# Kernel tuning notes

Hardware: AMD Instinct MI355X
Metric: run time of the kernel (lower is better)

Reference implementation:

```python
import jax, jax.numpy as jnp
import numpy as np

N = 16384   # total nodes (16 graphs x 32x32 grid)
E = 65536   # edges (before self loops)
F_IN = 7
H = 8       # gat heads
C = 200     # gat hidden per head
HC = H * C  # 1600
GCN = 1600
CNN = 64
OUT = 6
B = 16      # graphs per batch
G = 32      # grid size
EPS = 1e-5


def _bn1(x, g, b):
    # BatchNorm1d, training-mode batch stats (biased var), x: [N, F]
    mu = x.mean(0)
    var = x.var(0)
    return (x - mu) * jax.lax.rsqrt(var + EPS) * g + b


def _bn2(x, g, b):
    # BatchNorm2d over (N, H, W), x: [B, C, H, W]
    mu = x.mean((0, 2, 3), keepdims=True)
    var = x.var((0, 2, 3), keepdims=True)
    return (x - mu) * jax.lax.rsqrt(var + EPS) * g[None, :, None, None] + b[None, :, None, None]


def _conv5(x, w, b):
    y = jax.lax.conv_general_dilated(x, w, (1, 1), [(2, 2), (2, 2)],
                                     dimension_numbers=('NCHW', 'OIHW', 'NCHW'))
    return y + b[None, :, None, None]


def _gatv2(x, Wl, bl, Wr, br, We, att, bias, src, dst, edge_attr):
    # PyG GATv2Conv: concat=True, add_self_loops=True (fill_value='mean'), edge_dim=1
    n = x.shape[0]
    xl = (x @ Wl + bl).reshape(n, H, C)  # source transform
    xr = (x @ Wr + br).reshape(n, H, C)  # target transform
    loop = jnp.arange(n, dtype=src.dtype)
    s = jnp.concatenate([src, loop])
    d = jnp.concatenate([dst, loop])
    ea_loop = jnp.broadcast_to(edge_attr.mean(0, keepdims=True), (n, edge_attr.shape[1]))
    ea = jnp.concatenate([edge_attr, ea_loop], 0)
    ee = (ea @ We).reshape(-1, H, C)
    m = jax.nn.leaky_relu(xl[s] + xr[d] + ee, 0.2)       # [E+N, H, C]
    alpha = jnp.einsum('ehc,hc->eh', m, att)             # [E+N, H]
    amax = jax.ops.segment_max(alpha, d, num_segments=n)
    ex = jnp.exp(alpha - amax[d])
    denom = jax.ops.segment_sum(ex, d, num_segments=n)
    a = ex / denom[d]                                    # scatter-softmax over in-edges
    out = jax.ops.segment_sum(xl[s] * a[:, :, None], d, num_segments=n)  # [N, H, C]
    return out.reshape(n, HC) + bias


def setup_inputs() -> dict:
    k = jax.random.key(0)
    ks = jax.random.split(k, 16)
    def nrm(i, shape, s):
        return jax.random.normal(ks[i], shape, jnp.float32) * s
    z = lambda *s: jnp.zeros(s, jnp.float32)
    o = lambda *s: jnp.ones(s, jnp.float32)
    return {
        'x': nrm(0, (N, F_IN), 1.0),
        'edge_attr': jax.random.uniform(ks[1], (E, 1), jnp.float32),
        'Wl': nrm(2, (F_IN, HC), 0.3), 'bl': z(HC),
        'Wr': nrm(3, (F_IN, HC), 0.3), 'br': z(HC),
        'We': nrm(4, (1, HC), 0.3), 'att': nrm(5, (H, C), 0.1), 'gat_b': z(HC),
        'bn1_g': o(HC), 'bn1_b': z(HC),
        'W1': nrm(6, (HC, GCN), 0.025), 'b1': z(GCN),
        'bn2_g': o(GCN), 'bn2_b': z(GCN),
        'W2': nrm(7, (GCN, GCN), 0.025), 'b2': z(GCN),
        'Wp': nrm(8, (GCN, CNN), 0.025), 'bp': z(CNN),
        'cw1': nrm(9, (CNN, CNN, 5, 5), 0.025), 'cb1': z(CNN), 'g1': o(CNN), 'be1': z(CNN),
        'cw2': nrm(10, (128, CNN, 5, 5), 0.025), 'cb2': z(128), 'g2': o(128), 'be2': z(128),
        'cw3': nrm(11, (CNN, 128, 5, 5), 0.025), 'cb3': z(CNN), 'g3': o(CNN), 'be3': z(CNN),
        'cw4': nrm(12, (OUT, CNN, 5, 5), 0.025), 'cb4': z(OUT),
        'src': jax.random.randint(ks[13], (E,), 0, N, jnp.int32),
        'dst': jax.random.randint(ks[14], (E,), 0, N, jnp.int32),
    }


def reference(x, edge_attr, Wl, bl, Wr, br, We, att, gat_b, bn1_g, bn1_b,
              W1, b1, bn2_g, bn2_b, W2, b2, Wp, bp,
              cw1, cb1, g1, be1, cw2, cb2, g2, be2, cw3, cb3, g3, be3, cw4, cb4,
              src, dst):
    h = _gatv2(x, Wl, bl, Wr, br, We, att, gat_b, src, dst, edge_attr)
    h = jax.nn.leaky_relu(_bn1(h, bn1_g, bn1_b), 0.01)
    h = jax.nn.relu(_bn1(h @ W1 + b1, bn2_g, bn2_b))
    h = jax.nn.relu(h @ W2 + b2)
    # per-graph projection + reshape to grid (batch vector is contiguous arange//1024)
    h = (h @ Wp + bp).reshape(B, G, G, CNN).transpose(0, 3, 1, 2)  # [B, CNN, G, G]
    h = jax.nn.relu(_bn2(_conv5(h, cw1, cb1), g1, be1))
    h = jax.nn.relu(_bn2(_conv5(h, cw2, cb2), g2, be2))
    h = jax.nn.relu(_bn2(_conv5(h, cw3, cb3), g3, be3))
    return _conv5(h, cw4, cb4)  # [B, 6, G, G]
```

## Files before the change

kernel.cpp:

```cpp
#include <hip/hip_runtime.h>
#include <cstdint>
#include <cstddef>

#define N_NODES 16384
#define N_EDGES 65536
#define EN_TOT  (N_EDGES + N_NODES)
#define FIN 7
#define HC 1600
#define NH 8
#define CHD 200
#define GCN 1600
#define CNN 64
#define BATCH 16
#define BN_EPS 1e-5f

typedef unsigned short ushort_t;
typedef __attribute__((ext_vector_type(8))) short s8frag;
typedef __attribute__((ext_vector_type(4))) float f32x4;

__device__ __forceinline__ ushort_t f2bf(float f) {
    unsigned u = __float_as_uint(f);
    unsigned r = (u + 0x7FFFu + ((u >> 16) & 1u)) >> 16;
    return (ushort_t)r;
}
__device__ __forceinline__ float bf2f(ushort_t u) {
    return __uint_as_float(((unsigned)u) << 16);
}

__device__ __forceinline__ void gload16(const void* g, void* l) {
    __builtin_amdgcn_global_load_lds((const __attribute__((address_space(1))) void*)g,
                                     (__attribute__((address_space(3))) void*)l, 16, 0, 0);
}

#define SWZ_KOFF(tid) ((((tid) & 3) ^ (((tid) >> 3) & 3)) << 3)
#define SWZ_AQ(lane, am) (((((lane) >> 4) ^ (((am) >> 1) & 3)) << 3))

__global__ __launch_bounds__(256) void k_count(
    const int* __restrict__ dst, const float* __restrict__ ea,
    int* __restrict__ cnt, float* __restrict__ ea_sum)
{
    int e = blockIdx.x * 256 + threadIdx.x;
    int d = (e < N_EDGES) ? dst[e] : (e - N_EDGES);
    atomicAdd(&cnt[d], 1);
    float v = (e < N_EDGES) ? ea[e] : 0.f;
#pragma unroll
    for (int o = 1; o < 64; o <<= 1) v += __shfl_xor(v, o);
    if ((threadIdx.x & 63) == 0) atomicAdd(ea_sum, v);
}

__global__ __launch_bounds__(256) void k_scan(int* __restrict__ cnt, int* __restrict__ offs)
{
    __shared__ int part[256];
    int t = threadIdx.x;
    int base_i = t * 64;
    int s = 0;
    for (int i = 0; i < 64; i++) s += cnt[base_i + i];
    part[t] = s;
    __syncthreads();
    for (int o = 1; o < 256; o <<= 1) {
        int add = (t >= o) ? part[t - o] : 0;
        __syncthreads();
        part[t] += add;
        __syncthreads();
    }
    int run = (t == 0) ? 0 : part[t - 1];
    for (int i = 0; i < 64; i++) {
        int v = cnt[base_i + i];
        offs[base_i + i] = run;
        run += v;
        cnt[base_i + i] = 0;
    }
    if (t == 255) offs[N_NODES] = run;
}

__global__ __launch_bounds__(256) void k_fill(const int* __restrict__ dst,
    const int* __restrict__ offs, int* __restrict__ cur, int* __restrict__ eid)
{
    int e = blockIdx.x * 256 + threadIdx.x;
    if (e >= EN_TOT) return;
    int d = (e < N_EDGES) ? dst[e] : (e - N_EDGES);
    int pos = offs[d] + atomicAdd(&cur[d], 1);
    eid[pos] = e;
}

__global__ __launch_bounds__(256) void k_gprep(
    const float* __restrict__ Wl, const float* __restrict__ bl,
    const float* __restrict__ Wr, const float* __restrict__ br,
    const float* __restrict__ We, const float* __restrict__ att,
    ushort_t* __restrict__ G, float* __restrict__ att16)
{
    int cp = blockIdx.x * 256 + threadIdx.x;
    if (cp >= 8 * 208) return;
    int h = cp / 208, j = cp - h * 208;
    ushort_t v[32];
#pragma unroll
    for (int k = 0; k < 32; k++) v[k] = 0;
    float av = 0.f;
    if (j < 200) {
        int c = h * 200 + j;
#pragma unroll
        for (int k = 0; k < 7; k++) v[k]     = f2bf(Wl[k * HC + c]);
#pragma unroll
        for (int k = 0; k < 7; k++) v[7 + k] = f2bf(Wr[k * HC + c]);
        v[14] = f2bf(We[c]);
        v[15] = f2bf(bl[c] + br[c]);
        av = att[h * CHD + j];
    }
    uint4* dst4 = (uint4*)(G + (size_t)cp * 32);
#pragma unroll
    for (int i = 0; i < 4; i++) dst4[i] = ((uint4*)v)[i];
    att16[cp] = av;
}

__global__ __launch_bounds__(256) void k_alpha_mm(
    const float* __restrict__ x, const float* __restrict__ edge_attr,
    const float* __restrict__ ea_sum, const int* __restrict__ src,
    const int* __restrict__ dst, const ushort_t* __restrict__ G,
    const float* __restrict__ att16, float* __restrict__ alpha)
{
    __shared__ ushort_t Fs[64 * 32];
    int tid = threadIdx.x;
    int lane = tid & 63, w = tid >> 6;
    int e0 = blockIdx.x * 64;
    float eam = ea_sum[0] * (1.f / (float)N_EDGES);

#define FSLOT(j, k) ((j) * 32 + ((((k) >> 3) ^ (((j) >> 1) & 3)) << 3) + ((k) & 7))
    for (int i = tid; i < 64 * 16; i += 256) {
        int j = i >> 4, k = (i & 15) + 16;
        Fs[FSLOT(j, k)] = 0;
    }
    {
        int j = tid >> 2, part = tid & 3;
        int e = e0 + j;
        int s, d; float ea;
        if (e < N_EDGES) { s = src[e]; d = dst[e]; ea = edge_attr[e]; }
        else             { s = e - N_EDGES; d = s; ea = eam; }
        if (part == 0) {
#pragma unroll
            for (int k = 0; k < 4; k++) Fs[FSLOT(j, k)] = f2bf(x[s * 7 + k]);
        } else if (part == 1) {
#pragma unroll
            for (int k = 4; k < 7; k++) Fs[FSLOT(j, k)] = f2bf(x[s * 7 + k]);
            Fs[FSLOT(j, 7)] = f2bf(x[d * 7 + 0]);
        } else if (part == 2) {
#pragma unroll
            for (int k = 1; k < 5; k++) Fs[FSLOT(j, 7 + k)] = f2bf(x[d * 7 + k]);
        } else {
            Fs[FSLOT(j, 12)] = f2bf(x[d * 7 + 5]);
            Fs[FSLOT(j, 13)] = f2bf(x[d * 7 + 6]);
            Fs[FSLOT(j, 14)] = f2bf(ea);
            Fs[FSLOT(j, 15)] = f2bf(1.0f);
        }
    }
#undef FSLOT
    __syncthreads();

    int am = lane & 15;
    int aq = (lane >> 4) * 8;
    s8frag afrag = *(const s8frag*)&Fs[(w * 16 + am) * 32 + SWZ_AQ(lane, am)];
    int lr4 = (lane >> 4) * 4;
    int ew = e0 + w * 16;
#pragma unroll
    for (int h = 0; h < NH; h++) {
        f32x4 hacc = (f32x4)0.f;
        int colbase = h * 208;
#pragma unroll
        for (int t = 0; t < 13; t++) {
            int cb = colbase + t * 16;
            s8frag bfrag = *(const s8frag*)(G + ((size_t)(cb + am) * 32 + aq));
            f32x4 z = (f32x4)0.f;
            f32x4 p = __builtin_amdgcn_mfma_f32_16x16x32_bf16(afrag, bfrag, z, 0, 0, 0);
            float attv = att16[cb + am];
#pragma unroll
            for (int r = 0; r < 4; r++) {
                float v = p[r];
                v = (v >= 0.f) ? v : 0.2f * v;
                hacc[r] += v * attv;
            }
        }
#pragma unroll
        for (int o = 1; o <= 8; o <<= 1) {
#pragma unroll
            for (int r = 0; r < 4; r++) hacc[r] += __shfl_xor(hacc[r], o);
        }
        if (am == 0) {
#pragma unroll
            for (int r = 0; r < 4; r++)
                alpha[(size_t)(ew + lr4 + r) * NH + h] = hacc[r];
        }
    }
}

__global__ __launch_bounds__(256) void k_agg_x(
    const float* __restrict__ x, const float* __restrict__ alpha,
    const int* __restrict__ offs, const int* __restrict__ eid,
    const int* __restrict__ src, float* __restrict__ xbar)
{
    int n = blockIdx.x * 4 + (threadIdx.x >> 6);
    int lane = threadIdx.x & 63;
    int beg = offs[n], deg = offs[n + 1] - beg;

    float pm[NH];
#pragma unroll
    for (int h = 0; h < NH; h++) pm[h] = -1e30f;
    for (int j = lane; j < deg; j += 64) {
        int e = eid[beg + j];
        const float* ap = alpha + (size_t)e * NH;
#pragma unroll
        for (int h = 0; h < NH; h++) pm[h] = fmaxf(pm[h], ap[h]);
    }
#pragma unroll
    for (int h = 0; h < NH; h++)
#pragma unroll
        for (int o = 1; o < 64; o <<= 1)
            pm[h] = fmaxf(pm[h], __shfl_xor(pm[h], o));

    float ps[NH];
    float px[NH][7];
#pragma unroll
    for (int h = 0; h < NH; h++) {
        ps[h] = 0.f;
#pragma unroll
        for (int k = 0; k < 7; k++) px[h][k] = 0.f;
    }
    for (int j = lane; j < deg; j += 64) {
        int e = eid[beg + j];
        int s = (e < N_EDGES) ? src[e] : (e - N_EDGES);
        float xv[7];
#pragma unroll
        for (int k = 0; k < 7; k++) xv[k] = x[s * 7 + k];
        const float* ap = alpha + (size_t)e * NH;
#pragma unroll
        for (int h = 0; h < NH; h++) {
            float p = __expf(ap[h] - pm[h]);
            ps[h] += p;
#pragma unroll
            for (int k = 0; k < 7; k++) px[h][k] += p * xv[k];
        }
    }
#pragma unroll
    for (int h = 0; h < NH; h++) {
#pragma unroll
        for (int o = 1; o < 64; o <<= 1) ps[h] += __shfl_xor(ps[h], o);
#pragma unroll
        for (int k = 0; k < 7; k++)
#pragma unroll
            for (int o = 1; o < 64; o <<= 1) px[h][k] += __shfl_xor(px[h][k], o);
    }
    float val = 0.f;
#pragma unroll
    for (int h = 0; h < NH; h++)
#pragma unroll
        for (int k = 0; k < 7; k++)
            if (lane == h * 7 + k) val = px[h][k] / ps[h];
    if (lane < 56) xbar[(size_t)n * 56 + lane] = val;
}

__global__ __launch_bounds__(256) void k_xmom(
    const float* __restrict__ xbar, float* __restrict__ mom)
{
    int h = blockIdx.x & 7, chunk = blockIdx.x >> 3;
    int tid = threadIdx.x, lane = tid & 63;
    float mu[7], S[49];
#pragma unroll
    for (int k = 0; k < 7; k++) mu[k] = 0.f;
#pragma unroll
    for (int k = 0; k < 49; k++) S[k] = 0.f;
    for (int i = 0; i < 8; i++) {
        int n = chunk * 2048 + i * 256 + tid;
        const float* xb = xbar + (size_t)n * 56 + h * 7;
        float xv[7];
#pragma unroll
        for (int k = 0; k < 7; k++) xv[k] = xb[k];
#pragma unroll
        for (int k = 0; k < 7; k++) {
            mu[k] += xv[k];
#pragma unroll
            for (int kk = 0; kk < 7; kk++) S[k * 7 + kk] += xv[k] * xv[kk];
        }
    }
#pragma unroll
    for (int o = 1; o < 64; o <<= 1) {
#pragma unroll
        for (int k = 0; k < 7; k++) mu[k] += __shfl_xor(mu[k], o);
#pragma unroll
        for (int k = 0; k < 49; k++) S[k] += __shfl_xor(S[k], o);
    }
    if (lane == 0) {
        float* mh = mom + h * 56;
#pragma unroll
        for (int k = 0; k < 7; k++) atomicAdd(&mh[k], mu[k]);
#pragma unroll
        for (int k = 0; k < 49; k++) atomicAdd(&mh[7 + k], S[k]);
    }
}

__global__ __launch_bounds__(256) void k_bn1_prep(
    const float* __restrict__ mom, const float* __restrict__ Wl,
    const float* __restrict__ bl, const float* __restrict__ gat_b,
    const float* __restrict__ g, const float* __restrict__ b,
    float* __restrict__ scale, float* __restrict__ shift)
{
    int f = blockIdx.x * 256 + threadIdx.x;
    if (f >= HC) return;
    int h = f / CHD;
    const float* mh = mom + h * 56;
    const float inv = 1.f / (float)N_NODES;
    float m[7], w[7];
#pragma unroll
    for (int k = 0; k < 7; k++) {
        m[k] = mh[k] * inv;
        w[k] = Wl[k * HC + f];
    }
    float mean = bl[f] + gat_b[f];
#pragma unroll
    for (int k = 0; k < 7; k++) mean += w[k] * m[k];
    float var = 0.f;
#pragma unroll
    for (int k = 0; k < 7; k++)
#pragma unroll
        for (int kk = 0; kk < 7; kk++)
            var += w[k] * w[kk] * (mh[7 + k * 7 + kk] * inv - m[k] * m[kk]);
    var = fmaxf(var, 0.f);
    float sc = g[f] * rsqrtf(var + BN_EPS);
    scale[f] = sc;
    shift[f] = b[f] - mean * sc;
}

__global__ __launch_bounds__(256) void k_project_bn(
    const float* __restrict__ xbar, const float* __restrict__ Wl,
    const float* __restrict__ bl, const float* __restrict__ gat_b,
    const float* __restrict__ scale, const float* __restrict__ shift,
    ushort_t* __restrict__ hout)
{
    __shared__ float xs[56];
    int n = blockIdx.x, tid = threadIdx.x;
    if (tid < 56) xs[tid] = xbar[(size_t)n * 56 + tid];
    __syncthreads();
    if (tid >= 200) return;
    int f0 = tid * 8;
    int h = f0 / CHD;
    float xb[7];
#pragma unroll
    for (int k = 0; k < 7; k++) xb[k] = xs[h * 7 + k];
    float acc[8];
    {
        float4 b0 = *(const float4*)(bl + f0), b1 = *(const float4*)(bl + f0 + 4);
        float4 g0 = *(const float4*)(gat_b + f0), g1 = *(const float4*)(gat_b + f0 + 4);
        acc[0] = b0.x + g0.x; acc[1] = b0.y + g0.y; acc[2] = b0.z + g0.z; acc[3] = b0.w + g0.w;
        acc[4] = b1.x + g1.x; acc[5] = b1.y + g1.y; acc[6] = b1.z + g1.z; acc[7] = b1.w + g1.w;
    }
#pragma unroll
    for (int k = 0; k < 7; k++) {
        float4 w0 = *(const float4*)(Wl + k * HC + f0);
        float4 w1 = *(const float4*)(Wl + k * HC + f0 + 4);
        acc[0] += xb[k] * w0.x; acc[1] += xb[k] * w0.y;
        acc[2] += xb[k] * w0.z; acc[3] += xb[k] * w0.w;
        acc[4] += xb[k] * w1.x; acc[5] += xb[k] * w1.y;
        acc[6] += xb[k] * w1.z; acc[7] += xb[k] * w1.w;
    }
    float4 s0 = *(const float4*)(scale + f0), s1 = *(const float4*)(scale + f0 + 4);
    float4 h0 = *(const float4*)(shift + f0), h1 = *(const float4*)(shift + f0 + 4);
    float sc[8] = {s0.x, s0.y, s0.z, s0.w, s1.x, s1.y, s1.z, s1.w};
    float sh[8] = {h0.x, h0.y, h0.z, h0.w, h1.x, h1.y, h1.z, h1.w};
    ushort_t o[8];
#pragma unroll
    for (int i = 0; i < 8; i++) {
        float v = acc[i] * sc[i] + sh[i];
        v = (v >= 0.f) ? v : 0.01f * v;
        o[i] = f2bf(v);
    }
    *(uint4*)(hout + (size_t)n * HC + f0) = *(uint4*)o;
}

__global__ __launch_bounds__(256) void k_bn_apply_bb(
    const ushort_t* __restrict__ X, ushort_t* __restrict__ Y,
    const float* __restrict__ bsum, const float* __restrict__ bsq,
    const float* __restrict__ g, const float* __restrict__ b,
    int rows, int total8, int F)
{
    int idx = blockIdx.x * 256 + threadIdx.x;
    if (idx >= total8) return;
    int e0 = idx * 8;
    int f0 = e0 % F;
    float inv = 1.f / (float)rows;
    uint4 xin = *(const uint4*)(X + e0);
    ushort_t* xv = (ushort_t*)&xin;
    ushort_t o[8];
#pragma unroll
    for (int i = 0; i < 8; i += 4) {
        float4 su = *(const float4*)(bsum + f0 + i);
        float4 sq = *(const float4*)(bsq + f0 + i);
        float4 gg = *(const float4*)(g + f0 + i);
        float4 bb = *(const float4*)(b + f0 + i);
        float mu, var, sc, sh, v;
#define DO1(comp, j) \
        mu = su.comp * inv; var = sq.comp * inv - mu * mu; \
        sc = gg.comp * rsqrtf(var + BN_EPS); sh = bb.comp - mu * sc; \
        v = bf2f(xv[i + j]) * sc + sh; v = fmaxf(v, 0.f); o[i + j] = f2bf(v);
        DO1(x, 0) DO1(y, 1) DO1(z, 2) DO1(w, 3)
#undef DO1
    }
    *(uint4*)(Y + e0) = *(uint4*)o;
}

__global__ __launch_bounds__(256) void k_bn_apply_pad(
    const ushort_t* __restrict__ X, ushort_t* __restrict__ pad,
    const float* __restrict__ bsum, const float* __restrict__ bsq,
    const float* __restrict__ g, const float* __restrict__ b,
    int total8, int Csh)
{
    int idx = blockIdx.x * 256 + threadIdx.x;
    if (idx >= total8) return;
    int e0 = idx * 8;
    int C = 1 << Csh;
    int c0 = e0 & (C - 1);
    int pix = e0 >> Csh;
    int xx = pix & 31, yy = (pix >> 5) & 31, bb2 = pix >> 10;
    float inv = 1.f / 16384.f;
    uint4 xin = *(const uint4*)(X + e0);
    ushort_t* xv = (ushort_t*)&xin;
    ushort_t o[8];
#pragma unroll
    for (int i = 0; i < 8; i += 4) {
        float4 su = *(const float4*)(bsum + c0 + i);
        float4 sq = *(const float4*)(bsq + c0 + i);
        float4 gg = *(const float4*)(g + c0 + i);
        float4 bb = *(const float4*)(b + c0 + i);
        float mu, var, sc, sh, v;
#define DO1(comp, j) \
        mu = su.comp * inv; var = sq.comp * inv - mu * mu; \
        sc = gg.comp * rsqrtf(var + BN_EPS); sh = bb.comp - mu * sc; \
        v = bf2f(xv[i + j]) * sc + sh; v = fmaxf(v, 0.f); o[i + j] = f2bf(v);
        DO1(x, 0) DO1(y, 1) DO1(z, 2) DO1(w, 3)
#undef DO1
    }
    *(uint4*)(pad + (((size_t)((bb2 * 36 + yy + 2) * 36 + xx + 2)) << Csh) + c0) = *(uint4*)o;
}

__global__ __launch_bounds__(256) void k_wt(
    const float* __restrict__ W, ushort_t* __restrict__ BT, int Kdim, int Ndim, int Npad)
{
    __shared__ float t[32][33];
    int tx = threadIdx.x & 31, ty = threadIdx.x >> 5;
    int n0 = blockIdx.x * 32, k0 = blockIdx.y * 32;
#pragma unroll
    for (int i = 0; i < 4; i++)
        t[ty + i * 8][tx] = (n0 + tx < Ndim)
            ? W[(size_t)(k0 + ty + i * 8) * Ndim + n0 + tx] : 0.f;
    __syncthreads();
#pragma unroll
    for (int i = 0; i < 4; i++)
        BT[(size_t)(n0 + ty + i * 8) * Kdim + k0 + tx] = f2bf(t[tx][ty + i * 8]);
}

__global__ __launch_bounds__(256) void k_cwt_all(
    const float* __restrict__ w1, const float* __restrict__ w2,
    const float* __restrict__ w3, const float* __restrict__ w4,
    ushort_t* __restrict__ o1, ushort_t* __restrict__ o2,
    ushort_t* __restrict__ o3, ushort_t* __restrict__ o4)
{
    int idx = blockIdx.x * 256 + threadIdx.x;
    const int R1 = 128 * 1600, R2 = 128 * 1600, R3 = 128 * 3200;
    const float* w; ushort_t* o; int local, K, Cin, Cout;
    if (idx < R1)                { w = w1; o = o1; local = idx; K = 1600; Cin = 64;  Cout = 64; }
    else if (idx < R1 + R2)      { w = w2; o = o2; local = idx - R1; K = 1600; Cin = 64; Cout = 128; }
    else if (idx < R1 + R2 + R3) { w = w3; o = o3; local = idx - R1 - R2; K = 3200; Cin = 128; Cout = 64; }
    else                         { w = w4; o = o4; local = idx - R1 - R2 - R3; K = 1600; Cin = 64; Cout = 6; }
    int co = local / K;
    int k = local - co * K;
    int p = k / Cin, ci = k - p * Cin;
    o[local] = (co < Cout) ? f2bf(w[(size_t)(co * Cin + ci) * 25 + p]) : (ushort_t)0;
}

__global__ __launch_bounds__(256) void k_mgemm(
    const ushort_t* __restrict__ A, const ushort_t* __restrict__ BT,
    const float* __restrict__ bias, ushort_t* __restrict__ Cb,
    float* __restrict__ bsum, float* __restrict__ bsq,
    int K, int Nvalid, int ldc, int relu)
{
    __shared__ __align__(16) ushort_t As[128 * 64];
    __shared__ __align__(16) ushort_t Bs[128 * 64];
    int tid = threadIdx.x;
    int lane = tid & 63;
    int wid = tid >> 6;
    int wy = wid >> 1, wx = wid & 1;

    int nx = gridDim.x;
    int lin = blockIdx.y * nx + blockIdx.x;
    int xcd = lin & 7;
    int q = lin >> 3;
    int colb = q % nx;
    int rowb = (q / nx) * 8 + xcd;
    int row0 = rowb * 128, col0 = colb * 128;

    f32x4 acc[4][4];
#pragma unroll
    for (int i = 0; i < 4; i++)
#pragma unroll
        for (int j = 0; j < 4; j++) acc[i][j] = (f32x4)0.f;

    int am = lane & 15, qq = lane >> 4;
    int lr4 = qq * 4;

    const ushort_t* pA[4];
    const ushort_t* pB[4];
    char* lA[4];
    char* lB[4];
#pragma unroll
    for (int j = 0; j < 4; j++) {
        int sA = j * 256 + tid;
        int rowS = sA >> 3, cS = sA & 7;
        int srcC = (cS ^ (rowS & 7)) << 3;
        pA[j] = A  + (size_t)(row0 + rowS) * K + srcC;
        pB[j] = BT + (size_t)(col0 + rowS) * K + srcC;
        lA[j] = (char*)As + sA * 16;
        lB[j] = (char*)Bs + sA * 16;
    }

    for (int kk = 0; kk < K; kk += 64) {
        __syncthreads();
#pragma unroll
        for (int j = 0; j < 4; j++) {
            gload16(pA[j], lA[j]); pA[j] += 64;
            gload16(pB[j], lB[j]); pB[j] += 64;
        }
        __syncthreads();

#pragma unroll
        for (int t = 0; t < 2; t++) {
            int sw = ((((t << 2) | qq) ^ (am & 7)) << 3);
            s8frag a[4], b[4];
#pragma unroll
            for (int mi = 0; mi < 4; mi++)
                a[mi] = *(const s8frag*)&As[(wy * 64 + mi * 16 + am) * 64 + sw];
#pragma unroll
            for (int ni = 0; ni < 4; ni++)
                b[ni] = *(const s8frag*)&Bs[(wx * 64 + ni * 16 + am) * 64 + sw];
#pragma unroll
            for (int mi = 0; mi < 4; mi++)
#pragma unroll
                for (int ni = 0; ni < 4; ni++)
                    acc[mi][ni] = __builtin_amdgcn_mfma_f32_16x16x32_bf16(
                        a[mi], b[ni], acc[mi][ni], 0, 0, 0);
        }
    }

    int lc = am;
#pragma unroll
    for (int ni = 0; ni < 4; ni++) {
        int col = col0 + wx * 64 + ni * 16 + lc;
        bool valid = col < Nvalid;
        float bv = valid ? bias[col] : 0.f;
        float s = 0.f, q2 = 0.f;
#pragma unroll
        for (int mi = 0; mi < 4; mi++) {
#pragma unroll
            for (int r = 0; r < 4; r++) {
                int row = row0 + wy * 64 + mi * 16 + lr4 + r;
                float v = acc[mi][ni][r] + bv;
                s += v; q2 += v * v;
                float vo = relu ? fmaxf(v, 0.f) : v;
                if (valid) Cb[(size_t)row * ldc + col] = f2bf(vo);
            }
        }
        if (bsum != nullptr && valid) {
            s += __shfl_xor(s, 16);  s += __shfl_xor(s, 32);
            q2 += __shfl_xor(q2, 16); q2 += __shfl_xor(q2, 32);
            if (qq == 0) {
                atomicAdd(&bsum[col], s);
                atomicAdd(&bsq[col], q2);
            }
        }
    }
}

__global__ __launch_bounds__(256) void k_cgemm3(
    const ushort_t* __restrict__ Ain, const ushort_t* __restrict__ BT,
    const float* __restrict__ bias, float* __restrict__ Cf, ushort_t* __restrict__ Cb,
    float* __restrict__ bsum, float* __restrict__ bsq,
    int K, int Csh, int Nvalid, int ldc, int out_mode, int linA)
{
    __shared__ __align__(16) ushort_t As[32 * 64];
    __shared__ __align__(16) ushort_t Bs[64 * 64];
    int tid = threadIdx.x;
    int lane = tid & 63;
    int w = tid >> 6, wr = w >> 1, wc = w & 1;
    int row0 = blockIdx.y * 32, col0 = blockIdx.x * 64;
    int Cmask = (1 << Csh) - 1;

    f32x4 acc[2];
    acc[0] = (f32x4)0.f; acc[1] = (f32x4)0.f;

    int rowSA = tid >> 3, cSA = tid & 7;
    int srcCA = (cSA ^ (rowSA & 7)) << 3;
    int pixA = row0 + rowSA;
    int bA = pixA >> 10, yA = (pixA >> 5) & 31, xA = pixA & 31;
    const ushort_t* aptr = Ain + (size_t)pixA * K + srcCA;

    int rowSB0 = tid >> 3, rowSB1 = rowSB0 + 32;
    int cSB = tid & 7;
    const ushort_t* bptr0 = BT + (size_t)(col0 + rowSB0) * K + ((cSB ^ (rowSB0 & 7)) << 3);
    const ushort_t* bptr1 = BT + (size_t)(col0 + rowSB1) * K + ((cSB ^ (rowSB1 & 7)) << 3);

    char* lA  = (char*)As + tid * 16;
    char* lB0 = (char*)Bs + tid * 16;
    char* lB1 = (char*)Bs + (tid + 256) * 16;

    int am = lane & 15, qq = lane >> 4;

    for (int kk = 0; kk < K; kk += 64) {
        __syncthreads();
        if (linA) {
            gload16(aptr, lA);
            aptr += 64;
        } else {
            int k = kk + srcCA;
            int p = k >> Csh;
            int ci = k & Cmask;
            int ky = p / 5, kx = p - ky * 5;
            gload16(Ain + (((size_t)((bA * 36 + yA + ky) * 36 + xA + kx) << Csh) + ci), lA);
        }
        gload16(bptr0, lB0); bptr0 += 64;
        gload16(bptr1, lB1); bptr1 += 64;
        __syncthreads();

#pragma unroll
        for (int t = 0; t < 2; t++) {
            int sw = ((((t << 2) | qq) ^ (am & 7)) << 3);
            s8frag a   = *(const s8frag*)&As[(wr * 16 + am) * 64 + sw];
            s8frag b0f = *(const s8frag*)&Bs[(wc * 32 + am) * 64 + sw];
            s8frag b1f = *(const s8frag*)&Bs[(wc * 32 + 16 + am) * 64 + sw];
            acc[0] = __builtin_amdgcn_mfma_f32_16x16x32_bf16(a, b0f, acc[0], 0, 0, 0);
            acc[1] = __builtin_amdgcn_mfma_f32_16x16x32_bf16(a, b1f, acc[1], 0, 0, 0);
        }
    }

    int lc = am, lr4 = qq * 4;
#pragma unroll
    for (int ni = 0; ni < 2; ni++) {
        int col = col0 + wc * 32 + ni * 16 + lc;
        bool valid = col < Nvalid;
        float bv = valid ? bias[col] : 0.f;
        float s = 0.f, q2 = 0.f;
#pragma unroll
        for (int r = 0; r < 4; r++) {
            int row = row0 + wr * 16 + lr4 + r;
            float v = acc[ni][r] + bv;
            s += v; q2 += v * v;
            if (valid) {
                if (out_mode == 1) {
                    Cb[(size_t)row * ldc + col] = f2bf(v);
                } else if (out_mode == 3) {
                    int bb = row >> 10, sp = row & 1023;
                    int yy = sp >> 5, xx = sp & 31;
                    Cb[((size_t)((bb * 36 + yy + 2) * 36 + xx + 2) << 6) + col] = f2bf(v);
                } else {
                    int bb = row >> 10, sp = row & 1023;
                    Cf[(size_t)((bb * 6 + col) << 10) + sp] = v;
                }
            }
        }
        if (bsum != nullptr && valid) {
            s += __shfl_xor(s, 16);  s += __shfl_xor(s, 32);
            q2 += __shfl_xor(q2, 16); q2 += __shfl_xor(q2, 32);
            if (qq == 0) {
                atomicAdd(&bsum[col], s);
                atomicAdd(&bsq[col], q2);
            }
        }
    }
}

extern "C" void kernel_launch(void* const* d_in, const int* in_sizes, int n_in,
                              void* d_out, int out_size, void* d_ws, size_t ws_size,
                              hipStream_t stream)
{
    const float* x   = (const float*)d_in[0];
    const float* ea  = (const float*)d_in[1];
    const float* Wl  = (const float*)d_in[2];
    const float* bl  = (const float*)d_in[3];
    const float* Wr  = (const float*)d_in[4];
    const float* br  = (const float*)d_in[5];
    const float* We  = (const float*)d_in[6];
    const float* att = (const float*)d_in[7];
    const float* gat_b = (const float*)d_in[8];
    const float* bn1_g = (const float*)d_in[9];
    const float* bn1_b = (const float*)d_in[10];
    const float* W1 = (const float*)d_in[11];
    const float* b1 = (const float*)d_in[12];
    const float* bn2_g = (const float*)d_in[13];
    const float* bn2_b = (const float*)d_in[14];
    const float* W2 = (const float*)d_in[15];
    const float* b2 = (const float*)d_in[16];
    const float* Wp = (const float*)d_in[17];
    const float* bp = (const float*)d_in[18];
    const float* cw1 = (const float*)d_in[19]; const float* cb1 = (const float*)d_in[20];
    const float* g1  = (const float*)d_in[21]; const float* be1 = (const float*)d_in[22];
    const float* cw2 = (const float*)d_in[23]; const float* cb2 = (const float*)d_in[24];
    const float* g2  = (const float*)d_in[25]; const float* be2 = (const float*)d_in[26];
    const float* cw3 = (const float*)d_in[27]; const float* cb3 = (const float*)d_in[28];
    const float* g3  = (const float*)d_in[29]; const float* be3 = (const float*)d_in[30];
    const float* cw4 = (const float*)d_in[31]; const float* cb4 = (const float*)d_in[32];
    const int* src = (const int*)d_in[33];
    const int* dst = (const int*)d_in[34];
    float* out = (float*)d_out;

    const size_t SZ_REGION = (size_t)N_NODES * HC * 4;
    const size_t HALF = SZ_REGION / 2;
    char* ws = (char*)d_ws;
    char* regA = ws;
    char* regB = regA + SZ_REGION;
    char* wbase = regB + SZ_REGION;
    ushort_t* W1T  = (ushort_t*)wbase;
    ushort_t* W2T  = W1T + (size_t)1664 * 1600;
    ushort_t* WpT  = W2T + (size_t)1664 * 1600;
    ushort_t* c1T  = WpT + (size_t)128 * 1600;
    ushort_t* c2T  = c1T + (size_t)128 * 1600;
    ushort_t* c3T  = c2T + (size_t)128 * 1600;
    ushort_t* c4T  = c3T + (size_t)128 * 3200;
    ushort_t* G16  = c4T + (size_t)128 * 1600;
    float* att16   = (float*)(G16 + (size_t)1664 * 32);
    float* alpha   = att16 + 1664 + 64;
    float* xbar    = alpha + (size_t)EN_TOT * NH;
    float* bn_sc   = xbar + (size_t)N_NODES * 56;
    float* bn_sh   = bn_sc + HC;
    int*   cnt    = (int*)(bn_sh + HC + 64);
    float* ea_sum = (float*)(cnt + N_NODES);
    float* mom    = ea_sum + 16;
    float* bnG1   = mom + 448;
    float* bnC1   = bnG1 + 3200;
    float* bnC2   = bnC1 + 256;
    float* bnC3   = bnC2 + 256;
    const size_t ZBYTES = (char*)(bnC3 + 256) - (char*)cnt;
    int* offs = (int*)(bnC3 + 256 + 16);
    int* eid  = offs + N_NODES + 1 + 63;

    ushort_t* abuf16  = (ushort_t*)regA;
    ushort_t* a2buf16 = (ushort_t*)(regA + HALF);
    ushort_t* pad1 = (ushort_t*)regA;
    ushort_t* pad2 = (ushort_t*)(regA + (4u << 20));
    ushort_t* pad3 = (ushort_t*)(regA + (8u << 20));
    ushort_t* pad4 = (ushort_t*)(regA + (14u << 20));
    ushort_t* c1out = (ushort_t*)(regA + (18u << 20));
    ushort_t* c2out = (ushort_t*)(regA + (22u << 20));
    ushort_t* c3out = (ushort_t*)(regA + (27u << 20));
    ushort_t* g1b16   = (ushort_t*)regB;
    ushort_t* h3_16   = (ushort_t*)regB;

    k_wt<<<dim3(52, 50), 256, 0, stream>>>(W1, W1T, 1600, 1600, 1664);
    k_wt<<<dim3(52, 50), 256, 0, stream>>>(W2, W2T, 1600, 1600, 1664);
    k_wt<<<dim3(4, 50), 256, 0, stream>>>(Wp, WpT, 1600, 64, 128);
    k_cwt_all<<<4000, 256, 0, stream>>>(cw1, cw2, cw3, cw4, c1T, c2T, c3T, c4T);
    k_gprep<<<7, 256, 0, stream>>>(Wl, bl, Wr, br, We, att, G16, att16);

    hipMemsetAsync(cnt, 0, ZBYTES, stream);
    k_count<<<EN_TOT / 256, 256, 0, stream>>>(dst, ea, cnt, ea_sum);
    k_scan<<<1, 256, 0, stream>>>(cnt, offs);
    k_fill<<<EN_TOT / 256, 256, 0, stream>>>(dst, offs, cnt, eid);
    k_alpha_mm<<<EN_TOT / 64, 256, 0, stream>>>(x, ea, ea_sum, src, dst, G16, att16, alpha);
    k_agg_x<<<N_NODES / 4, 256, 0, stream>>>(x, alpha, offs, eid, src, xbar);

    k_xmom<<<64, 256, 0, stream>>>(xbar, mom);
    k_bn1_prep<<<7, 256, 0, stream>>>(mom, Wl, bl, gat_b, bn1_g, bn1_b, bn_sc, bn_sh);
    k_project_bn<<<N_NODES, 256, 0, stream>>>(xbar, Wl, bl, gat_b, bn_sc, bn_sh, abuf16);

    k_mgemm<<<dim3(13, 128), 256, 0, stream>>>(abuf16, W1T, b1, g1b16,
                                               bnG1, bnG1 + 1600, 1600, 1600, 1600, 0);
    k_bn_apply_bb<<<(N_NODES * GCN / 8) / 256, 256, 0, stream>>>(g1b16, a2buf16,
                                                                 bnG1, bnG1 + 1600, bn2_g, bn2_b,
                                                                 N_NODES, N_NODES * GCN / 8, GCN);
    k_mgemm<<<dim3(13, 128), 256, 0, stream>>>(a2buf16, W2T, b2, h3_16,
                                               (float*)nullptr, (float*)nullptr, 1600, 1600, 1600, 1);

    hipMemsetAsync(regA, 0, (size_t)17 << 20, stream);

    k_cgemm3<<<dim3(1, 512), 256, 0, stream>>>(h3_16, WpT, bp, (float*)nullptr, pad1,
                                               (float*)nullptr, (float*)nullptr,
                                               1600, 6, 64, 64, 3, 1);
    k_cgemm3<<<dim3(1, 512), 256, 0, stream>>>(pad1, c1T, cb1, (float*)nullptr, c1out,
                                               bnC1, bnC1 + 128, 1600, 6, 64, 64, 1, 0);
    k_bn_apply_pad<<<(16384 * 64 / 8) / 256, 256, 0, stream>>>(c1out, pad2, bnC1, bnC1 + 128,
                                                               g1, be1, 16384 * 64 / 8, 6);
    k_cgemm3<<<dim3(2, 512), 256, 0, stream>>>(pad2, c2T, cb2, (float*)nullptr, c2out,
                                               bnC2, bnC2 + 128, 1600, 6, 128, 128, 1, 0);
    k_bn_apply_pad<<<(16384 * 128 / 8) / 256, 256, 0, stream>>>(c2out, pad3, bnC2, bnC2 + 128,
                                                                g2, be2, 16384 * 128 / 8, 7);
    k_cgemm3<<<dim3(1, 512), 256, 0, stream>>>(pad3, c3T, cb3, (float*)nullptr, c3out,
                                               bnC3, bnC3 + 128, 3200, 7, 64, 64, 1, 0);
    k_bn_apply_pad<<<(16384 * 64 / 8) / 256, 256, 0, stream>>>(c3out, pad4, bnC3, bnC3 + 128,
                                                               g3, be3, 16384 * 64 / 8, 6);
    k_cgemm3<<<dim3(1, 512), 256, 0, stream>>>(pad4, c4T, cb4, out, (ushort_t*)nullptr,
                                               (float*)nullptr, (float*)nullptr,
                                               1600, 6, 6, 6, 2, 0);

    (void)in_sizes; (void)n_in; (void)out_size; (void)ws_size;
}
```

Baseline: 843.7 us.

## Fuse CNN stage into one cooperative kernel and merge weight-prep launches

Replaces the four conv GEMM launches and three BN-apply launches with a single cooperative kernel of 512 blocks. Each block keeps its conv accumulators in registers across a grid.sync, then applies batch-norm and ReLU and writes straight into the next padded buffer, so the intermediate conv outputs are never written to or read back from memory. All weight-transpose and prep kernels are also merged into one launch. The cost is several grid-wide barriers, a layer-2 block that now computes both 64-column halves serially instead of spreading them over twice as many blocks, and a dependence on all 512 blocks being co-resident.

```diff
diff --git a/kernel.cpp b/kernel.cpp
--- a/kernel.cpp
+++ b/kernel.cpp
@@ -1,6 +1,9 @@
 #include <hip/hip_runtime.h>
+#include <hip/hip_cooperative_groups.h>
 #include <cstdint>
 #include <cstddef>
+
+namespace cg = cooperative_groups;
 
 #define N_NODES 16384
 #define N_EDGES 65536
@@ -83,33 +86,72 @@
     eid[pos] = e;
 }
 
-__global__ __launch_bounds__(256) void k_gprep(
+__global__ __launch_bounds__(256) void k_prep(
+    const float* __restrict__ W1, const float* __restrict__ W2, const float* __restrict__ Wp,
+    const float* __restrict__ cw1, const float* __restrict__ cw2,
+    const float* __restrict__ cw3, const float* __restrict__ cw4,
     const float* __restrict__ Wl, const float* __restrict__ bl,
     const float* __restrict__ Wr, const float* __restrict__ br,
     const float* __restrict__ We, const float* __restrict__ att,
+    ushort_t* __restrict__ W1T, ushort_t* __restrict__ W2T, ushort_t* __restrict__ WpT,
+    ushort_t* __restrict__ c1T, ushort_t* __restrict__ c2T,
+    ushort_t* __restrict__ c3T, ushort_t* __restrict__ c4T,
     ushort_t* __restrict__ G, float* __restrict__ att16)
 {
-    int cp = blockIdx.x * 256 + threadIdx.x;
-    if (cp >= 8 * 208) return;
-    int h = cp / 208, j = cp - h * 208;
-    ushort_t v[32];
-#pragma unroll
-    for (int k = 0; k < 32; k++) v[k] = 0;
-    float av = 0.f;
-    if (j < 200) {
-        int c = h * 200 + j;
-#pragma unroll
-        for (int k = 0; k < 7; k++) v[k]     = f2bf(Wl[k * HC + c]);
-#pragma unroll
-        for (int k = 0; k < 7; k++) v[7 + k] = f2bf(Wr[k * HC + c]);
-        v[14] = f2bf(We[c]);
-        v[15] = f2bf(bl[c] + br[c]);
-        av = att[h * CHD + j];
-    }
-    uint4* dst4 = (uint4*)(G + (size_t)cp * 32);
-#pragma unroll
-    for (int i = 0; i < 4; i++) dst4[i] = ((uint4*)v)[i];
-    att16[cp] = av;
+    __shared__ float t[32][33];
+    int lb = blockIdx.x;
+    int tid = threadIdx.x;
+    if (lb < 5400) {
+        const float* W; ushort_t* BT; int Ndim, bx, by;
+        if (lb < 2600)      { W = W1; BT = W1T; Ndim = 1600; bx = lb % 52; by = lb / 52; }
+        else if (lb < 5200) { W = W2; BT = W2T; Ndim = 1600; int l = lb - 2600; bx = l % 52; by = l / 52; }
+        else                { W = Wp; BT = WpT; Ndim = 64;   int l = lb - 5200; bx = l % 4;  by = l / 4; }
+        int tx = tid & 31, ty = tid >> 5;
+        int n0 = bx * 32, k0 = by * 32;
+#pragma unroll
+        for (int i = 0; i < 4; i++)
+            t[ty + i * 8][tx] = (n0 + tx < Ndim)
+                ? W[(size_t)(k0 + ty + i * 8) * Ndim + n0 + tx] : 0.f;
+        __syncthreads();
+#pragma unroll
+        for (int i = 0; i < 4; i++)
+            BT[(size_t)(n0 + ty + i * 8) * 1600 + k0 + tx] = f2bf(t[tx][ty + i * 8]);
+    } else if (lb < 9400) {
+        int idx = (lb - 5400) * 256 + tid;
+        const int R1 = 128 * 1600, R2 = 128 * 1600, R3 = 128 * 3200;
+        const float* w; ushort_t* o; int local, K, Cin, Cout;
+        if (idx < R1)                { w = cw1; o = c1T; local = idx; K = 1600; Cin = 64;  Cout = 64; }
+        else if (idx < R1 + R2)      { w = cw2; o = c2T; local = idx - R1; K = 1600; Cin = 64; Cout = 128; }
+        else if (idx < R1 + R2 + R3) { w = cw3; o = c3T; local = idx - R1 - R2; K = 3200; Cin = 128; Cout = 64; }
+        else                         { w = cw4; o = c4T; local = idx - R1 - R2 - R3; K = 1600; Cin = 64; Cout = 6; }
+        int co = local / K;
+        int k = local - co * K;
+        int p = k / Cin, ci = k - p * Cin;
+        o[local] = (co < Cout) ? f2bf(w[(size_t)(co * Cin + ci) * 25 + p]) : (ushort_t)0;
+    } else {
+        int cp = (lb - 9400) * 256 + tid;
+        if (cp < 8 * 208) {
+            int h = cp / 208, j = cp - h * 208;
+            ushort_t v[32];
+#pragma unroll
+            for (int k = 0; k < 32; k++) v[k] = 0;
+            float av = 0.f;
+            if (j < 200) {
+                int c = h * 200 + j;
+#pragma unroll
+                for (int k = 0; k < 7; k++) v[k]     = f2bf(Wl[k * HC + c]);
+#pragma unroll
+                for (int k = 0; k < 7; k++) v[7 + k] = f2bf(Wr[k * HC + c]);
+                v[14] = f2bf(We[c]);
+                v[15] = f2bf(bl[c] + br[c]);
+                av = att[h * CHD + j];
+            }
+            uint4* dst4 = (uint4*)(G + (size_t)cp * 32);
+#pragma unroll
+            for (int i = 0; i < 4; i++) dst4[i] = ((uint4*)v)[i];
+            att16[cp] = av;
+        }
+    }
 }
 
 __global__ __launch_bounds__(256) void k_alpha_mm(
@@ -404,75 +446,6 @@
     *(uint4*)(Y + e0) = *(uint4*)o;
 }
 
-__global__ __launch_bounds__(256) void k_bn_apply_pad(
-    const ushort_t* __restrict__ X, ushort_t* __restrict__ pad,
-    const float* __restrict__ bsum, const float* __restrict__ bsq,
-    const float* __restrict__ g, const float* __restrict__ b,
-    int total8, int Csh)
-{
-    int idx = blockIdx.x * 256 + threadIdx.x;
-    if (idx >= total8) return;
-    int e0 = idx * 8;
-    int C = 1 << Csh;
-    int c0 = e0 & (C - 1);
-    int pix = e0 >> Csh;
-    int xx = pix & 31, yy = (pix >> 5) & 31, bb2 = pix >> 10;
-    float inv = 1.f / 16384.f;
-    uint4 xin = *(const uint4*)(X + e0);
-    ushort_t* xv = (ushort_t*)&xin;
-    ushort_t o[8];
-#pragma unroll
-    for (int i = 0; i < 8; i += 4) {
-        float4 su = *(const float4*)(bsum + c0 + i);
-        float4 sq = *(const float4*)(bsq + c0 + i);
-        float4 gg = *(const float4*)(g + c0 + i);
-        float4 bb = *(const float4*)(b + c0 + i);
-        float mu, var, sc, sh, v;
-#define DO1(comp, j) \
-        mu = su.comp * inv; var = sq.comp * inv - mu * mu; \
-        sc = gg.comp * rsqrtf(var + BN_EPS); sh = bb.comp - mu * sc; \
-        v = bf2f(xv[i + j]) * sc + sh; v = fmaxf(v, 0.f); o[i + j] = f2bf(v);
-        DO1(x, 0) DO1(y, 1) DO1(z, 2) DO1(w, 3)
-#undef DO1
-    }
-    *(uint4*)(pad + (((size_t)((bb2 * 36 + yy + 2) * 36 + xx + 2)) << Csh) + c0) = *(uint4*)o;
-}
-
-__global__ __launch_bounds__(256) void k_wt(
-    const float* __restrict__ W, ushort_t* __restrict__ BT, int Kdim, int Ndim, int Npad)
-{
-    __shared__ float t[32][33];
-    int tx = threadIdx.x & 31, ty = threadIdx.x >> 5;
-    int n0 = blockIdx.x * 32, k0 = blockIdx.y * 32;
-#pragma unroll
-    for (int i = 0; i < 4; i++)
-        t[ty + i * 8][tx] = (n0 + tx < Ndim)
-            ? W[(size_t)(k0 + ty + i * 8) * Ndim + n0 + tx] : 0.f;
-    __syncthreads();
-#pragma unroll
-    for (int i = 0; i < 4; i++)
-        BT[(size_t)(n0 + ty + i * 8) * Kdim + k0 + tx] = f2bf(t[tx][ty + i * 8]);
-}
-
-__global__ __launch_bounds__(256) void k_cwt_all(
-    const float* __restrict__ w1, const float* __restrict__ w2,
-    const float* __restrict__ w3, const float* __restrict__ w4,
-    ushort_t* __restrict__ o1, ushort_t* __restrict__ o2,
-    ushort_t* __restrict__ o3, ushort_t* __restrict__ o4)
-{
-    int idx = blockIdx.x * 256 + threadIdx.x;
-    const int R1 = 128 * 1600, R2 = 128 * 1600, R3 = 128 * 3200;
-    const float* w; ushort_t* o; int local, K, Cin, Cout;
-    if (idx < R1)                { w = w1; o = o1; local = idx; K = 1600; Cin = 64;  Cout = 64; }
-    else if (idx < R1 + R2)      { w = w2; o = o2; local = idx - R1; K = 1600; Cin = 64; Cout = 128; }
-    else if (idx < R1 + R2 + R3) { w = w3; o = o3; local = idx - R1 - R2; K = 3200; Cin = 128; Cout = 64; }
-    else                         { w = w4; o = o4; local = idx - R1 - R2 - R3; K = 1600; Cin = 64; Cout = 6; }
-    int co = local / K;
-    int k = local - co * K;
-    int p = k / Cin, ci = k - p * Cin;
-    o[local] = (co < Cout) ? f2bf(w[(size_t)(co * Cin + ci) * 25 + p]) : (ushort_t)0;
-}
-
 __global__ __launch_bounds__(256) void k_mgemm(
     const ushort_t* __restrict__ A, const ushort_t* __restrict__ BT,
     const float* __restrict__ bias, ushort_t* __restrict__ Cb,
@@ -575,21 +548,25 @@
     }
 }
 
-__global__ __launch_bounds__(256) void k_cgemm3(
+struct CArgs {
+    const ushort_t *h3, *WpT, *c1T, *c2T, *c3T, *c4T;
+    const float *bp, *cb1, *cb2, *cb3, *cb4;
+    const float *g1, *be1, *g2, *be2, *g3, *be3;
+    float *bnC1, *bnC2, *bnC3;
+    ushort_t *pad1, *pad2, *pad3, *pad4;
+    float *out;
+};
+
+__device__ __forceinline__ void gemm_tile32x64(
     const ushort_t* __restrict__ Ain, const ushort_t* __restrict__ BT,
-    const float* __restrict__ bias, float* __restrict__ Cf, ushort_t* __restrict__ Cb,
-    float* __restrict__ bsum, float* __restrict__ bsq,
-    int K, int Csh, int Nvalid, int ldc, int out_mode, int linA)
-{
-    __shared__ __align__(16) ushort_t As[32 * 64];
-    __shared__ __align__(16) ushort_t Bs[64 * 64];
+    int K, int Csh, int linA, int row0, int col0,
+    ushort_t* As, ushort_t* Bs, f32x4* acc)
+{
     int tid = threadIdx.x;
     int lane = tid & 63;
+    int am = lane & 15, qq = lane >> 4;
     int w = tid >> 6, wr = w >> 1, wc = w & 1;
-    int row0 = blockIdx.y * 32, col0 = blockIdx.x * 64;
     int Cmask = (1 << Csh) - 1;
-
-    f32x4 acc[2];
     acc[0] = (f32x4)0.f; acc[1] = (f32x4)0.f;
 
     int rowSA = tid >> 3, cSA = tid & 7;
@@ -607,24 +584,19 @@
     char* lB0 = (char*)Bs + tid * 16;
     char* lB1 = (char*)Bs + (tid + 256) * 16;
 
-    int am = lane & 15, qq = lane >> 4;
-
     for (int kk = 0; kk < K; kk += 64) {
         __syncthreads();
         if (linA) {
-            gload16(aptr, lA);
-            aptr += 64;
+            gload16(aptr, lA); aptr += 64;
         } else {
             int k = kk + srcCA;
-            int p = k >> Csh;
-            int ci = k & Cmask;
+            int p = k >> Csh, ci = k & Cmask;
             int ky = p / 5, kx = p - ky * 5;
             gload16(Ain + (((size_t)((bA * 36 + yA + ky) * 36 + xA + kx) << Csh) + ci), lA);
         }
         gload16(bptr0, lB0); bptr0 += 64;
         gload16(bptr1, lB1); bptr1 += 64;
         __syncthreads();
-
 #pragma unroll
         for (int t = 0; t < 2; t++) {
             int sw = ((((t << 2) | qq) ^ (am & 7)) << 3);
@@ -635,39 +607,118 @@
             acc[1] = __builtin_amdgcn_mfma_f32_16x16x32_bf16(a, b1f, acc[1], 0, 0, 0);
         }
     }
-
-    int lc = am, lr4 = qq * 4;
+}
+
+__device__ __forceinline__ void stats_contrib(
+    const f32x4* acc, const float* bias, int col0, float* bsum, float* bsq)
+{
+    int lane = threadIdx.x & 63;
+    int am = lane & 15, qq = lane >> 4;
+    int wc = (threadIdx.x >> 6) & 1;
 #pragma unroll
     for (int ni = 0; ni < 2; ni++) {
-        int col = col0 + wc * 32 + ni * 16 + lc;
-        bool valid = col < Nvalid;
-        float bv = valid ? bias[col] : 0.f;
+        int col = col0 + wc * 32 + ni * 16 + am;
+        float bv = bias[col];
         float s = 0.f, q2 = 0.f;
 #pragma unroll
         for (int r = 0; r < 4; r++) {
-            int row = row0 + wr * 16 + lr4 + r;
             float v = acc[ni][r] + bv;
             s += v; q2 += v * v;
-            if (valid) {
-                if (out_mode == 1) {
-                    Cb[(size_t)row * ldc + col] = f2bf(v);
-                } else if (out_mode == 3) {
-                    int bb = row >> 10, sp = row & 1023;
-                    int yy = sp >> 5, xx = sp & 31;
-                    Cb[((size_t)((bb * 36 + yy + 2) * 36 + xx + 2) << 6) + col] = f2bf(v);
-                } else {
-                    int bb = row >> 10, sp = row & 1023;
-                    Cf[(size_t)((bb * 6 + col) << 10) + sp] = v;
-                }
-            }
-        }
-        if (bsum != nullptr && valid) {
-            s += __shfl_xor(s, 16);  s += __shfl_xor(s, 32);
-            q2 += __shfl_xor(q2, 16); q2 += __shfl_xor(q2, 32);
-            if (qq == 0) {
-                atomicAdd(&bsum[col], s);
-                atomicAdd(&bsq[col], q2);
-            }
+        }
+        s += __shfl_xor(s, 16);  s += __shfl_xor(s, 32);
+        q2 += __shfl_xor(q2, 16); q2 += __shfl_xor(q2, 32);
+        if (qq == 0) {
+            atomicAdd(&bsum[col], s);
+            atomicAdd(&bsq[col], q2);
+        }
+    }
+}
+
+__device__ __forceinline__ void apply_write_pad(
+    const f32x4* acc, const float* bias, const float* bsum, const float* bsq,
+    const float* g, const float* be, int row0, int col0, int Csh, ushort_t* pad)
+{
+    int lane = threadIdx.x & 63;
+    int am = lane & 15, qq = lane >> 4;
+    int w = threadIdx.x >> 6, wr = w >> 1, wc = w & 1;
+    const float inv = 1.f / 16384.f;
+#pragma unroll
+    for (int ni = 0; ni < 2; ni++) {
+        int col = col0 + wc * 32 + ni * 16 + am;
+        float mu = bsum[col] * inv;
+        float var = bsq[col] * inv - mu * mu;
+        float sc = g[col] * rsqrtf(var + BN_EPS);
+        float sh = be[col] - mu * sc;
+        float bv = bias[col];
+#pragma unroll
+        for (int r = 0; r < 4; r++) {
+            int row = row0 + wr * 16 + qq * 4 + r;
+            int bb = row >> 10, sp = row & 1023;
+            int yy = sp >> 5, xx = sp & 31;
+            float v = fmaxf((acc[ni][r] + bv) * sc + sh, 0.f);
+            pad[((size_t)((bb * 36 + yy + 2) * 36 + xx + 2) << Csh) + col] = f2bf(v);
+        }
+    }
+}
+
+__global__ __launch_bounds__(256) void k_convnet(CArgs a)
+{
+    cg::grid_group grid = cg::this_grid();
+    __shared__ __align__(16) ushort_t As[32 * 64];
+    __shared__ __align__(16) ushort_t Bs[64 * 64];
+    int row0 = blockIdx.x * 32;
+    int lane = threadIdx.x & 63;
+    int am = lane & 15, qq = lane >> 4;
+    int w = threadIdx.x >> 6, wr = w >> 1, wc = w & 1;
+    f32x4 acc[2], acc2[2];
+
+    gemm_tile32x64(a.h3, a.WpT, 1600, 6, 1, row0, 0, As, Bs, acc);
+#pragma unroll
+    for (int ni = 0; ni < 2; ni++) {
+        int col = wc * 32 + ni * 16 + am;
+        float bv = a.bp[col];
+#pragma unroll
+        for (int r = 0; r < 4; r++) {
+            int row = row0 + wr * 16 + qq * 4 + r;
+            int bb = row >> 10, sp = row & 1023;
+            int yy = sp >> 5, xx = sp & 31;
+            a.pad1[((size_t)((bb * 36 + yy + 2) * 36 + xx + 2) << 6) + col] = f2bf(acc[ni][r] + bv);
+        }
+    }
+    grid.sync();
+
+    gemm_tile32x64(a.pad1, a.c1T, 1600, 6, 0, row0, 0, As, Bs, acc);
+    stats_contrib(acc, a.cb1, 0, a.bnC1, a.bnC1 + 64);
+    grid.sync();
+    apply_write_pad(acc, a.cb1, a.bnC1, a.bnC1 + 64, a.g1, a.be1, row0, 0, 6, a.pad2);
+    grid.sync();
+
+    gemm_tile32x64(a.pad2, a.c2T, 1600, 6, 0, row0, 0,  As, Bs, acc);
+    gemm_tile32x64(a.pad2, a.c2T, 1600, 6, 0, row0, 64, As, Bs, acc2);
+    stats_contrib(acc,  a.cb2, 0,  a.bnC2, a.bnC2 + 128);
+    stats_contrib(acc2, a.cb2, 64, a.bnC2, a.bnC2 + 128);
+    grid.sync();
+    apply_write_pad(acc,  a.cb2, a.bnC2, a.bnC2 + 128, a.g2, a.be2, row0, 0,  7, a.pad3);
+    apply_write_pad(acc2, a.cb2, a.bnC2, a.bnC2 + 128, a.g2, a.be2, row0, 64, 7, a.pad3);
+    grid.sync();
+
+    gemm_tile32x64(a.pad3, a.c3T, 3200, 7, 0, row0, 0, As, Bs, acc);
+    stats_contrib(acc, a.cb3, 0, a.bnC3, a.bnC3 + 64);
+    grid.sync();
+    apply_write_pad(acc, a.cb3, a.bnC3, a.bnC3 + 64, a.g3, a.be3, row0, 0, 6, a.pad4);
+    grid.sync();
+
+    gemm_tile32x64(a.pad4, a.c4T, 1600, 6, 0, row0, 0, As, Bs, acc);
+#pragma unroll
+    for (int ni = 0; ni < 2; ni++) {
+        int col = wc * 32 + ni * 16 + am;
+        bool valid = col < 6;
+        float bv = valid ? a.cb4[col] : 0.f;
+#pragma unroll
+        for (int r = 0; r < 4; r++) {
+            int row = row0 + wr * 16 + qq * 4 + r;
+            int bb = row >> 10, sp = row & 1023;
+            if (valid) a.out[(size_t)((bb * 6 + col) << 10) + sp] = acc[ni][r] + bv;
         }
     }
 }
@@ -742,17 +793,12 @@
     ushort_t* pad2 = (ushort_t*)(regA + (4u << 20));
     ushort_t* pad3 = (ushort_t*)(regA + (8u << 20));
     ushort_t* pad4 = (ushort_t*)(regA + (14u << 20));
-    ushort_t* c1out = (ushort_t*)(regA + (18u << 20));
-    ushort_t* c2out = (ushort_t*)(regA + (22u << 20));
-    ushort_t* c3out = (ushort_t*)(regA + (27u << 20));
     ushort_t* g1b16   = (ushort_t*)regB;
     ushort_t* h3_16   = (ushort_t*)regB;
 
-    k_wt<<<dim3(52, 50), 256, 0, stream>>>(W1, W1T, 1600, 1600, 1664);
-    k_wt<<<dim3(52, 50), 256, 0, stream>>>(W2, W2T, 1600, 1600, 1664);
-    k_wt<<<dim3(4, 50), 256, 0, stream>>>(Wp, WpT, 1600, 64, 128);
-    k_cwt_all<<<4000, 256, 0, stream>>>(cw1, cw2, cw3, cw4, c1T, c2T, c3T, c4T);
-    k_gprep<<<7, 256, 0, stream>>>(Wl, bl, Wr, br, We, att, G16, att16);
+    k_prep<<<9407, 256, 0, stream>>>(W1, W2, Wp, cw1, cw2, cw3, cw4,
+                                     Wl, bl, Wr, br, We, att,
+                                     W1T, W2T, WpT, c1T, c2T, c3T, c4T, G16, att16);
 
     hipMemsetAsync(cnt, 0, ZBYTES, stream);
     k_count<<<EN_TOT / 256, 256, 0, stream>>>(dst, ea, cnt, ea_sum);
@@ -775,24 +821,15 @@
 
     hipMemsetAsync(regA, 0, (size_t)17 << 20, stream);
 
-    k_cgemm3<<<dim3(1, 512), 256, 0, stream>>>(h3_16, WpT, bp, (float*)nullptr, pad1,
-                                               (float*)nullptr, (float*)nullptr,
-                                               1600, 6, 64, 64, 3, 1);
-    k_cgemm3<<<dim3(1, 512), 256, 0, stream>>>(pad1, c1T, cb1, (float*)nullptr, c1out,
-                                               bnC1, bnC1 + 128, 1600, 6, 64, 64, 1, 0);
-    k_bn_apply_pad<<<(16384 * 64 / 8) / 256, 256, 0, stream>>>(c1out, pad2, bnC1, bnC1 + 128,
-                                                               g1, be1, 16384 * 64 / 8, 6);
-    k_cgemm3<<<dim3(2, 512), 256, 0, stream>>>(pad2, c2T, cb2, (float*)nullptr, c2out,
-                                               bnC2, bnC2 + 128, 1600, 6, 128, 128, 1, 0);
-    k_bn_apply_pad<<<(16384 * 128 / 8) / 256, 256, 0, stream>>>(c2out, pad3, bnC2, bnC2 + 128,
-                                                                g2, be2, 16384 * 128 / 8, 7);
-    k_cgemm3<<<dim3(1, 512), 256, 0, stream>>>(pad3, c3T, cb3, (float*)nullptr, c3out,
-                                               bnC3, bnC3 + 128, 3200, 7, 64, 64, 1, 0);
-    k_bn_apply_pad<<<(16384 * 64 / 8) / 256, 256, 0, stream>>>(c3out, pad4, bnC3, bnC3 + 128,
-                                                               g3, be3, 16384 * 64 / 8, 6);
-    k_cgemm3<<<dim3(1, 512), 256, 0, stream>>>(pad4, c4T, cb4, out, (ushort_t*)nullptr,
-                                               (float*)nullptr, (float*)nullptr,
-                                               1600, 6, 6, 6, 2, 0);
+    CArgs ca;
+    ca.h3 = h3_16; ca.WpT = WpT; ca.c1T = c1T; ca.c2T = c2T; ca.c3T = c3T; ca.c4T = c4T;
+    ca.bp = bp; ca.cb1 = cb1; ca.cb2 = cb2; ca.cb3 = cb3; ca.cb4 = cb4;
+    ca.g1 = g1; ca.be1 = be1; ca.g2 = g2; ca.be2 = be2; ca.g3 = g3; ca.be3 = be3;
+    ca.bnC1 = bnC1; ca.bnC2 = bnC2; ca.bnC3 = bnC3;
+    ca.pad1 = pad1; ca.pad2 = pad2; ca.pad3 = pad3; ca.pad4 = pad4;
+    ca.out = out;
+    void* kargs[] = { (void*)&ca };
+    hipLaunchCooperativeKernel((const void*)k_convnet, dim3(512), dim3(256), kargs, 0, stream);
 
     (void)in_sizes; (void)n_in; (void)out_size; (void)ws_size;
 }
```

Measured after the change: 1.235 ms. 1.46x slower.
